# Kernel optimization log

Hardware: AMD Instinct MI355X
Metric: run time of the kernel (lower is better)

The kernel has to match this reference:

```python
import jax, jax.numpy as jnp
import numpy as np

N_TOK = 2048      # flattened batch*seq tokens
D_MODEL = 1024    # in_features
D_INT = 512       # d_intermediate
N_EXPERTS = 8     # n_routed_experts
TOP_K = 2         # n_activated_experts


def setup_inputs() -> dict:
    key = jax.random.key(0)
    k1, k2, k3, k4, k5 = jax.random.split(key, 5)
    x = jax.random.normal(k1, (N_TOK, D_MODEL), dtype=jnp.float32)
    indices = jax.random.randint(k2, (N_TOK, TOP_K), 0, N_EXPERTS, dtype=jnp.int32)
    # router combine weights (normalized over top-k like a softmax router)
    weights = jax.nn.softmax(jax.random.normal(k3, (N_TOK, TOP_K), dtype=jnp.float32), axis=-1)
    # tokens-per-expert counts, consistent with indices (as the router would supply)
    counts = jnp.bincount(indices.reshape(-1), length=N_EXPERTS).astype(jnp.int32)
    # expert weights: fc1 -> 2*d_int (gated MLP), fc2 -> d_model; kaiming-ish scale
    s1 = 1.0 / np.sqrt(D_MODEL)
    s2 = 1.0 / np.sqrt(D_INT)
    fc1_weight = jax.random.uniform(k4, (N_EXPERTS, 2 * D_INT, D_MODEL), jnp.float32, -s1, s1)
    fc2_weight = jax.random.uniform(k5, (N_EXPERTS, D_MODEL, D_INT), jnp.float32, -s2, s2)
    return {"x": x, "weights": weights, "indices": indices, "counts": counts,
            "fc1_weight": fc1_weight, "fc2_weight": fc2_weight}


def reference(x, weights, indices, counts, fc1_weight, fc2_weight):
    # Dense dispatch-free formulation: run every token through every expert's
    # gated MLP, then gather the per-slot expert output. Identical math to the
    # sort / grouped-GEMM / scatter path for the selected (token, expert) pairs.
    # h: (n_tok, n_experts, 2*d_int)
    h = jnp.einsum('td,egd->teg', x, fc1_weight)
    y, z = jnp.split(h, 2, axis=-1)
    a = y * jax.nn.silu(z)  # GatedMLP: y * activation(z)
    # expert outputs: (n_tok, n_experts, d_model)
    out = jnp.einsum('tei,edi->ted', a, fc2_weight)
    # gather the chosen expert output for each of the top-k slots: (n_tok, k, d_model)
    per_slot = jnp.take_along_axis(out, indices[:, :, None], axis=1)
    # combine: z = bmm(weights[:, None], x_by_expert).squeeze(1)
    return jnp.einsum('tk,tkd->td', weights, per_slot)
```

## Files before the change

kernel.cpp:

```cpp
#include <hip/hip_runtime.h>

typedef unsigned short u16;
typedef unsigned int u32;
using short8  = __attribute__((ext_vector_type(8))) short;
using floatx4 = __attribute__((ext_vector_type(4))) float;

#define N_TOK   2048
#define D_MODEL 1024
#define D_INT   512
#define NE      8

#define O_TOK    0
#define O_WROW   24576
#define O_XG     65536
#define O_ACT    10551296
#define O_FC1B   36765696
#define O_FC2B   53542912

static __device__ inline u16 f2bf(float f) {
    u32 u = __builtin_bit_cast(u32, f);
    u = (u + 0x7fffu + ((u >> 16) & 1u)) >> 16;
    return (u16)u;
}
static __device__ inline u32 pack2(float a, float b) {
    return (u32)f2bf(a) | ((u32)f2bf(b) << 16);
}
static __device__ inline void glds16(const u16* g, u16* l) {
    __builtin_amdgcn_global_load_lds(
        (const __attribute__((address_space(1))) void*)g,
        (__attribute__((address_space(3))) void*)l, 16, 0, 0);
}

__global__ __launch_bounds__(256) void prep_kernel(
    const float* __restrict__ x, const float* __restrict__ wts,
    const int* __restrict__ indices, const int* __restrict__ counts,
    const float* __restrict__ fc1, u16* __restrict__ fc1b,
    u16* __restrict__ Xg, int* __restrict__ tok, float* __restrict__ wrow) {
    int b = blockIdx.x, tid = threadIdx.x;
    if (b < 4096) {
        size_t v = (size_t)b * 256 + tid;
        size_t off = v * 8;
        const floatx4* s4 = reinterpret_cast<const floatx4*>(fc1 + off);
        floatx4 a = s4[0], bb = s4[1];
        uint4 o;
        o.x = pack2(a[0], a[1]); o.y = pack2(a[2], a[3]);
        o.z = pack2(bb[0], bb[1]); o.w = pack2(bb[2], bb[3]);
        *reinterpret_cast<uint4*>(fc1b + off) = o;
        return;
    }
    {
        int t = b - 4096;
        int off[NE];
        {
            int acc = 0;
            #pragma unroll
            for (int e = 0; e < NE; e++) { off[e] = acc; acc += ((counts[e] + 63) >> 6) << 6; }
        }
        int e0 = indices[2 * t], e1 = indices[2 * t + 1];
        __shared__ int s0, s1;
        if (tid == 0) { s0 = 0; s1 = 0; }
        __syncthreads();
        int c0 = 0, c1 = 0;
        const int4* ip = reinterpret_cast<const int4*>(indices);
        #pragma unroll
        for (int i = 0; i < 4; i++) {
            int4 vv = ip[tid * 4 + i];
            int q = tid * 16 + i * 4;
            c0 += (q + 0 < 2 * t && vv.x == e0) + (q + 1 < 2 * t && vv.y == e0)
                + (q + 2 < 2 * t && vv.z == e0) + (q + 3 < 2 * t && vv.w == e0);
            c1 += (q + 0 <= 2 * t && vv.x == e1) + (q + 1 <= 2 * t && vv.y == e1)
                + (q + 2 <= 2 * t && vv.z == e1) + (q + 3 <= 2 * t && vv.w == e1);
        }
        if (c0) atomicAdd(&s0, c0);
        if (c1) atomicAdd(&s1, c1);
        __syncthreads();
        int r0 = off[e0] + s0;
        int r1 = off[e1] + s1;
        if (tid == 0) {
            tok[r0] = t; tok[r1] = t;
            wrow[r0] = wts[2 * t]; wrow[r1] = wts[2 * t + 1];
        }
        const floatx4* src = reinterpret_cast<const floatx4*>(x + (size_t)t * D_MODEL);
        floatx4 a = src[tid];
        uint2 o;
        o.x = pack2(a[0], a[1]); o.y = pack2(a[2], a[3]);
        *reinterpret_cast<uint2*>(Xg + (size_t)r0 * D_MODEL + tid * 4) = o;
        *reinterpret_cast<uint2*>(Xg + (size_t)r1 * D_MODEL + tid * 4) = o;
        return;
    }
}

static __device__ inline int xcd_swz576(int bid) {
    return (bid & 7) * 72 + (bid >> 3);
}

__global__ __launch_bounds__(256) void gemm1_kernel(
    const u16* __restrict__ Xg, const u16* __restrict__ fc1b,
    u16* __restrict__ Act, const int* __restrict__ counts,
    const float* __restrict__ fc2, u16* __restrict__ fc2b,
    float* __restrict__ out) {
    __shared__ u16 As[64 * 64];
    __shared__ u16 Bs[128 * 64];
    int tid = threadIdx.x;
    int b = blockIdx.x;
    if (b >= 576) {
        if (b < 2624) {
            size_t v = (size_t)(b - 576) * 256 + tid;
            size_t off = v * 8;
            const floatx4* s4 = reinterpret_cast<const floatx4*>(fc2 + off);
            floatx4 a = s4[0], bb = s4[1];
            uint4 o;
            o.x = pack2(a[0], a[1]); o.y = pack2(a[2], a[3]);
            o.z = pack2(bb[0], bb[1]); o.w = pack2(bb[2], bb[3]);
            *reinterpret_cast<uint4*>(fc2b + off) = o;
        } else {
            int z = b - 2624;
            floatx4* dst = reinterpret_cast<floatx4*>(out) + (size_t)z * 1024;
            #pragma unroll
            for (int i = 0; i < 4; i++) dst[i * 256 + tid] = (floatx4){0.f, 0.f, 0.f, 0.f};
        }
        return;
    }
    int soff[NE + 1];
    {
        int acc = 0;
        #pragma unroll
        for (int e2 = 0; e2 < NE; e2++) { soff[e2] = acc; acc += ((counts[e2] + 63) >> 6) << 6; }
        soff[NE] = acc;
    }
    int t = xcd_swz576(b);
    int bx = t & 7, by = t >> 3;
    int row0 = by * 64;
    if (row0 >= soff[NE]) return;
    int e = 0;
    while (soff[e + 1] <= row0) e++;
    const u16* A  = Xg + (size_t)row0 * 1024;
    const u16* Be = fc1b + (size_t)e * 1024 * 1024;

    int lane = tid & 63, w = tid >> 6;
    int m0 = (w >> 1) * 32, n0 = (w & 1) * 32;
    int lr = lane & 15, kq = lane >> 4;

    const u16* gA[2]; u16* lA[2];
    #pragma unroll
    for (int j = 0; j < 2; j++) {
        int v = tid + j * 256;
        int r = v >> 3, kb = (v & 7) ^ (r & 7);
        gA[j] = A + (size_t)r * 1024 + kb * 8;
        lA[j] = As + (w * 64 + j * 256) * 8;
    }
    const u16* gB[4]; u16* lB[4];
    #pragma unroll
    for (int j = 0; j < 4; j++) {
        int v = tid + j * 256;
        int r = v >> 3, kb = (v & 7) ^ (r & 7);
        int grow = (r < 64) ? (bx * 64 + r) : (448 + bx * 64 + r);
        gB[j] = Be + (size_t)grow * 1024 + kb * 8;
        lB[j] = Bs + (w * 64 + j * 256) * 8;
    }

    floatx4 aY[2][2], aZ[2][2];
    #pragma unroll
    for (int i = 0; i < 2; i++)
        #pragma unroll
        for (int j = 0; j < 2; j++) {
            aY[i][j] = (floatx4){0.f, 0.f, 0.f, 0.f};
            aZ[i][j] = (floatx4){0.f, 0.f, 0.f, 0.f};
        }

    for (int k0 = 0; k0 < 1024; k0 += 64) {
        glds16(gA[0] + k0, lA[0]); glds16(gA[1] + k0, lA[1]);
        glds16(gB[0] + k0, lB[0]); glds16(gB[1] + k0, lB[1]);
        glds16(gB[2] + k0, lB[2]); glds16(gB[3] + k0, lB[3]);
        __syncthreads();
        #pragma unroll
        for (int ks = 0; ks < 2; ks++) {
            int sw = ((ks * 4 + kq) ^ (lr & 7)) * 8;
            short8 af[2], by2[2], bz[2];
            #pragma unroll
            for (int i = 0; i < 2; i++)
                af[i] = *reinterpret_cast<const short8*>(&As[(m0 + i * 16 + lr) * 64 + sw]);
            #pragma unroll
            for (int j = 0; j < 2; j++) {
                by2[j] = *reinterpret_cast<const short8*>(&Bs[(n0 + j * 16 + lr) * 64 + sw]);
                bz[j]  = *reinterpret_cast<const short8*>(&Bs[(64 + n0 + j * 16 + lr) * 64 + sw]);
            }
            #pragma unroll
            for (int i = 0; i < 2; i++)
                #pragma unroll
                for (int j = 0; j < 2; j++) {
                    aY[i][j] = __builtin_amdgcn_mfma_f32_16x16x32_bf16(af[i], by2[j], aY[i][j], 0, 0, 0);
                    aZ[i][j] = __builtin_amdgcn_mfma_f32_16x16x32_bf16(af[i], bz[j], aZ[i][j], 0, 0, 0);
                }
        }
        __syncthreads();
    }
    #pragma unroll
    for (int i = 0; i < 2; i++)
        #pragma unroll
        for (int j = 0; j < 2; j++) {
            floatx4 y = aY[i][j], z = aZ[i][j];
            #pragma unroll
            for (int r = 0; r < 4; r++) {
                float zz = z[r];
                float av = y[r] * (zz / (1.0f + __expf(-zz)));
                int m = m0 + i * 16 + kq * 4 + r;
                int g = bx * 64 + n0 + j * 16 + lr;
                Act[(size_t)(row0 + m) * D_INT + g] = f2bf(av);
            }
        }
}

__global__ __launch_bounds__(256) void gemm2_kernel(
    const u16* __restrict__ Act, const u16* __restrict__ fc2b,
    float* __restrict__ out, const int* __restrict__ counts,
    const int* __restrict__ tok, const float* __restrict__ wrow) {
    __shared__ u16 As[64 * 64];
    __shared__ u16 Bs[128 * 64];
    __shared__ int sTok[64];
    __shared__ float sW[64];
    int tid = threadIdx.x;
    int soff[NE + 1];
    {
        int acc = 0;
        #pragma unroll
        for (int e2 = 0; e2 < NE; e2++) { soff[e2] = acc; acc += ((counts[e2] + 63) >> 6) << 6; }
        soff[NE] = acc;
    }
    int t = xcd_swz576(blockIdx.x);
    int bx = t & 7, by = t >> 3;
    int row0 = by * 64;
    if (row0 >= soff[NE]) return;
    int e = 0;
    while (soff[e + 1] <= row0) e++;
    const u16* A  = Act + (size_t)row0 * 512;
    const u16* Be = fc2b + (size_t)e * 1024 * 512;

    int lane = tid & 63, w = tid >> 6;
    int m0 = (w >> 1) * 32, n0 = (w & 1) * 64;
    int lr = lane & 15, kq = lane >> 4;

    const u16* gA[2]; u16* lA[2];
    #pragma unroll
    for (int j = 0; j < 2; j++) {
        int v = tid + j * 256;
        int r = v >> 3, kb = (v & 7) ^ (r & 7);
        gA[j] = A + (size_t)r * 512 + kb * 8;
        lA[j] = As + (w * 64 + j * 256) * 8;
    }
    const u16* gB[4]; u16* lB[4];
    #pragma unroll
    for (int j = 0; j < 4; j++) {
        int v = tid + j * 256;
        int r = v >> 3, kb = (v & 7) ^ (r & 7);
        gB[j] = Be + (size_t)(bx * 128 + r) * 512 + kb * 8;
        lB[j] = Bs + (w * 64 + j * 256) * 8;
    }

    floatx4 acc[2][4];
    #pragma unroll
    for (int i = 0; i < 2; i++)
        #pragma unroll
        for (int j = 0; j < 4; j++) acc[i][j] = (floatx4){0.f, 0.f, 0.f, 0.f};

    for (int k0 = 0; k0 < 512; k0 += 64) {
        glds16(gA[0] + k0, lA[0]); glds16(gA[1] + k0, lA[1]);
        glds16(gB[0] + k0, lB[0]); glds16(gB[1] + k0, lB[1]);
        glds16(gB[2] + k0, lB[2]); glds16(gB[3] + k0, lB[3]);
        __syncthreads();
        #pragma unroll
        for (int ks = 0; ks < 2; ks++) {
            int sw = ((ks * 4 + kq) ^ (lr & 7)) * 8;
            short8 af[2], bf[4];
            #pragma unroll
            for (int i = 0; i < 2; i++)
                af[i] = *reinterpret_cast<const short8*>(&As[(m0 + i * 16 + lr) * 64 + sw]);
            #pragma unroll
            for (int j = 0; j < 4; j++)
                bf[j] = *reinterpret_cast<const short8*>(&Bs[(n0 + j * 16 + lr) * 64 + sw]);
            #pragma unroll
            for (int i = 0; i < 2; i++)
                #pragma unroll
                for (int j = 0; j < 4; j++)
                    acc[i][j] = __builtin_amdgcn_mfma_f32_16x16x32_bf16(af[i], bf[j], acc[i][j], 0, 0, 0);
        }
        __syncthreads();
    }
    if (tid < 64) {
        int g = row0 + tid;
        bool val = (g - soff[e]) < counts[e];
        sTok[tid] = val ? tok[g] : -1;
        sW[tid]   = val ? wrow[g] : 0.f;
    }
    __syncthreads();
    #pragma unroll
    for (int i = 0; i < 2; i++)
        #pragma unroll
        for (int r = 0; r < 4; r++) {
            int m = m0 + i * 16 + kq * 4 + r;
            int tk = sTok[m];
            if (tk >= 0) {
                float wgt = sW[m];
                float* dst = out + (size_t)tk * D_MODEL + bx * 128;
                #pragma unroll
                for (int j = 0; j < 4; j++)
                    atomicAdd(dst + n0 + j * 16 + lr, wgt * acc[i][j][r]);
            }
        }
}

extern "C" void kernel_launch(void* const* d_in, const int* in_sizes, int n_in,
                              void* d_out, int out_size, void* d_ws, size_t ws_size,
                              hipStream_t stream) {
    const float* x       = (const float*)d_in[0];
    const float* wts     = (const float*)d_in[1];
    const int*   indices = (const int*)d_in[2];
    const int*   counts  = (const int*)d_in[3];
    const float* fc1     = (const float*)d_in[4];
    const float* fc2     = (const float*)d_in[5];
    float* out = (float*)d_out;
    char* ws = (char*)d_ws;

    int*   tok  = (int*)(ws + O_TOK);
    float* wrow = (float*)(ws + O_WROW);
    u16*   Xg   = (u16*)(ws + O_XG);
    u16*   Act  = (u16*)(ws + O_ACT);
    u16*   fc1b = (u16*)(ws + O_FC1B);
    u16*   fc2b = (u16*)(ws + O_FC2B);

    prep_kernel<<<6144, 256, 0, stream>>>(x, wts, indices, counts, fc1, fc1b,
                                          Xg, tok, wrow);
    gemm1_kernel<<<3136, 256, 0, stream>>>(Xg, fc1b, Act, counts, fc2, fc2b, out);
    gemm2_kernel<<<576, 256, 0, stream>>>(Act, fc2b, out, counts, tok, wrow);
}
```

Baseline: 147.2 us.

## Fuse prep, gemm1 and gemm2 into one persistent kernel with grid barriers

Replaces three kernel launches with a single persistent kernel of 576 blocks. The blocks grid-stride through the fc1 conversion and token dispatch, meet at a software grid barrier, run gemm1 while also converting fc2 and zeroing the output, meet at a second barrier, then run gemm2. The aim is to remove launch gaps and tail effects between stages. In exchange it adds a memset, relies on all 576 blocks being resident at once (the barrier deadlocks otherwise), and the barriers can cost more than the launches they replace.

```diff
diff --git a/kernel.cpp b/kernel.cpp
--- a/kernel.cpp
+++ b/kernel.cpp
@@ -9,9 +9,11 @@
 #define D_MODEL 1024
 #define D_INT   512
 #define NE      8
+#define NBLK    576
 
 #define O_TOK    0
 #define O_WROW   24576
+#define O_BAR    45056
 #define O_XG     65536
 #define O_ACT    10551296
 #define O_FC1B   36765696
@@ -31,81 +33,98 @@
         (__attribute__((address_space(3))) void*)l, 16, 0, 0);
 }
 
-__global__ __launch_bounds__(256) void prep_kernel(
+static __device__ inline void grid_barrier(int* c, int nblk) {
+    __syncthreads();
+    if (threadIdx.x == 0) {
+        __threadfence();
+        __hip_atomic_fetch_add(c, 1, __ATOMIC_RELEASE, __HIP_MEMORY_SCOPE_AGENT);
+        while (__hip_atomic_load(c, __ATOMIC_ACQUIRE, __HIP_MEMORY_SCOPE_AGENT) < nblk)
+            __builtin_amdgcn_s_sleep(1);
+        __threadfence();
+    }
+    __syncthreads();
+}
+
+static __device__ inline int xcd_swz576(int bid) {
+    return (bid & 7) * 72 + (bid >> 3);
+}
+
+__global__ __launch_bounds__(256, 4) void moe_fused(
     const float* __restrict__ x, const float* __restrict__ wts,
     const int* __restrict__ indices, const int* __restrict__ counts,
-    const float* __restrict__ fc1, u16* __restrict__ fc1b,
-    u16* __restrict__ Xg, int* __restrict__ tok, float* __restrict__ wrow) {
-    int b = blockIdx.x, tid = threadIdx.x;
-    if (b < 4096) {
-        size_t v = (size_t)b * 256 + tid;
-        size_t off = v * 8;
-        const floatx4* s4 = reinterpret_cast<const floatx4*>(fc1 + off);
-        floatx4 a = s4[0], bb = s4[1];
-        uint4 o;
-        o.x = pack2(a[0], a[1]); o.y = pack2(a[2], a[3]);
-        o.z = pack2(bb[0], bb[1]); o.w = pack2(bb[2], bb[3]);
-        *reinterpret_cast<uint4*>(fc1b + off) = o;
-        return;
-    }
-    {
-        int t = b - 4096;
-        int off[NE];
-        {
-            int acc = 0;
-            #pragma unroll
-            for (int e = 0; e < NE; e++) { off[e] = acc; acc += ((counts[e] + 63) >> 6) << 6; }
-        }
-        int e0 = indices[2 * t], e1 = indices[2 * t + 1];
-        __shared__ int s0, s1;
-        if (tid == 0) { s0 = 0; s1 = 0; }
-        __syncthreads();
-        int c0 = 0, c1 = 0;
-        const int4* ip = reinterpret_cast<const int4*>(indices);
-        #pragma unroll
-        for (int i = 0; i < 4; i++) {
-            int4 vv = ip[tid * 4 + i];
-            int q = tid * 16 + i * 4;
-            c0 += (q + 0 < 2 * t && vv.x == e0) + (q + 1 < 2 * t && vv.y == e0)
-                + (q + 2 < 2 * t && vv.z == e0) + (q + 3 < 2 * t && vv.w == e0);
-            c1 += (q + 0 <= 2 * t && vv.x == e1) + (q + 1 <= 2 * t && vv.y == e1)
-                + (q + 2 <= 2 * t && vv.z == e1) + (q + 3 <= 2 * t && vv.w == e1);
-        }
-        if (c0) atomicAdd(&s0, c0);
-        if (c1) atomicAdd(&s1, c1);
-        __syncthreads();
-        int r0 = off[e0] + s0;
-        int r1 = off[e1] + s1;
-        if (tid == 0) {
-            tok[r0] = t; tok[r1] = t;
-            wrow[r0] = wts[2 * t]; wrow[r1] = wts[2 * t + 1];
-        }
-        const floatx4* src = reinterpret_cast<const floatx4*>(x + (size_t)t * D_MODEL);
-        floatx4 a = src[tid];
-        uint2 o;
-        o.x = pack2(a[0], a[1]); o.y = pack2(a[2], a[3]);
-        *reinterpret_cast<uint2*>(Xg + (size_t)r0 * D_MODEL + tid * 4) = o;
-        *reinterpret_cast<uint2*>(Xg + (size_t)r1 * D_MODEL + tid * 4) = o;
-        return;
-    }
-}
-
-static __device__ inline int xcd_swz576(int bid) {
-    return (bid & 7) * 72 + (bid >> 3);
-}
-
-__global__ __launch_bounds__(256) void gemm1_kernel(
-    const u16* __restrict__ Xg, const u16* __restrict__ fc1b,
-    u16* __restrict__ Act, const int* __restrict__ counts,
-    const float* __restrict__ fc2, u16* __restrict__ fc2b,
-    float* __restrict__ out) {
+    const float* __restrict__ fc1, const float* __restrict__ fc2,
+    u16* __restrict__ fc1b, u16* __restrict__ fc2b,
+    u16* __restrict__ Xg, int* __restrict__ tok, float* __restrict__ wrow,
+    u16* __restrict__ Act, float* __restrict__ out, int* __restrict__ bar) {
     __shared__ u16 As[64 * 64];
     __shared__ u16 Bs[128 * 64];
+    __shared__ int sTok[64];
+    __shared__ float sW[64];
+    __shared__ int s0, s1;
+
     int tid = threadIdx.x;
-    int b = blockIdx.x;
-    if (b >= 576) {
-        if (b < 2624) {
-            size_t v = (size_t)(b - 576) * 256 + tid;
+    int bid = blockIdx.x;
+
+    int soff[NE + 1];
+    {
+        int acc = 0;
+        #pragma unroll
+        for (int e2 = 0; e2 < NE; e2++) { soff[e2] = acc; acc += ((counts[e2] + 63) >> 6) << 6; }
+        soff[NE] = acc;
+    }
+
+    for (int b = bid; b < 6144; b += NBLK) {
+        if (b < 4096) {
+            size_t v = (size_t)b * 256 + tid;
+            size_t off = v * 8;
+            const floatx4* s4 = reinterpret_cast<const floatx4*>(fc1 + off);
+            floatx4 a = s4[0], bb = s4[1];
+            uint4 o;
+            o.x = pack2(a[0], a[1]); o.y = pack2(a[2], a[3]);
+            o.z = pack2(bb[0], bb[1]); o.w = pack2(bb[2], bb[3]);
+            *reinterpret_cast<uint4*>(fc1b + off) = o;
+        } else {
+            int t = b - 4096;
+            int e0 = indices[2 * t], e1 = indices[2 * t + 1];
+            if (tid == 0) { s0 = 0; s1 = 0; }
+            __syncthreads();
+            int c0 = 0, c1 = 0;
+            const int4* ip = reinterpret_cast<const int4*>(indices);
+            #pragma unroll
+            for (int i = 0; i < 4; i++) {
+                int4 vv = ip[tid * 4 + i];
+                int q = tid * 16 + i * 4;
+                c0 += (q + 0 < 2 * t && vv.x == e0) + (q + 1 < 2 * t && vv.y == e0)
+                    + (q + 2 < 2 * t && vv.z == e0) + (q + 3 < 2 * t && vv.w == e0);
+                c1 += (q + 0 <= 2 * t && vv.x == e1) + (q + 1 <= 2 * t && vv.y == e1)
+                    + (q + 2 <= 2 * t && vv.z == e1) + (q + 3 <= 2 * t && vv.w == e1);
+            }
+            if (c0) atomicAdd(&s0, c0);
+            if (c1) atomicAdd(&s1, c1);
+            __syncthreads();
+            int r0 = soff[e0] + s0;
+            int r1 = soff[e1] + s1;
+            if (tid == 0) {
+                tok[r0] = t; tok[r1] = t;
+                wrow[r0] = wts[2 * t]; wrow[r1] = wts[2 * t + 1];
+            }
+            const floatx4* src = reinterpret_cast<const floatx4*>(x + (size_t)t * D_MODEL);
+            floatx4 a = src[tid];
+            uint2 o;
+            o.x = pack2(a[0], a[1]); o.y = pack2(a[2], a[3]);
+            *reinterpret_cast<uint2*>(Xg + (size_t)r0 * D_MODEL + tid * 4) = o;
+            *reinterpret_cast<uint2*>(Xg + (size_t)r1 * D_MODEL + tid * 4) = o;
+        }
+        __syncthreads();
+    }
+    grid_barrier(&bar[0], NBLK);
+
+    int lane = tid & 63, w = tid >> 6;
+    int lr = lane & 15, kq = lane >> 4;
+
+    for (int u = NBLK + bid; u < 3136; u += NBLK) {
+        if (u < 2624) {
+            size_t v = (size_t)(u - 576) * 256 + tid;
             size_t off = v * 8;
             const floatx4* s4 = reinterpret_cast<const floatx4*>(fc2 + off);
             floatx4 a = s4[0], bb = s4[1];
@@ -114,199 +133,175 @@
             o.z = pack2(bb[0], bb[1]); o.w = pack2(bb[2], bb[3]);
             *reinterpret_cast<uint4*>(fc2b + off) = o;
         } else {
-            int z = b - 2624;
+            int z = u - 2624;
             floatx4* dst = reinterpret_cast<floatx4*>(out) + (size_t)z * 1024;
             #pragma unroll
             for (int i = 0; i < 4; i++) dst[i * 256 + tid] = (floatx4){0.f, 0.f, 0.f, 0.f};
         }
-        return;
-    }
-    int soff[NE + 1];
+    }
     {
-        int acc = 0;
-        #pragma unroll
-        for (int e2 = 0; e2 < NE; e2++) { soff[e2] = acc; acc += ((counts[e2] + 63) >> 6) << 6; }
-        soff[NE] = acc;
-    }
-    int t = xcd_swz576(b);
-    int bx = t & 7, by = t >> 3;
-    int row0 = by * 64;
-    if (row0 >= soff[NE]) return;
-    int e = 0;
-    while (soff[e + 1] <= row0) e++;
-    const u16* A  = Xg + (size_t)row0 * 1024;
-    const u16* Be = fc1b + (size_t)e * 1024 * 1024;
-
-    int lane = tid & 63, w = tid >> 6;
-    int m0 = (w >> 1) * 32, n0 = (w & 1) * 32;
-    int lr = lane & 15, kq = lane >> 4;
-
-    const u16* gA[2]; u16* lA[2];
-    #pragma unroll
-    for (int j = 0; j < 2; j++) {
-        int v = tid + j * 256;
-        int r = v >> 3, kb = (v & 7) ^ (r & 7);
-        gA[j] = A + (size_t)r * 1024 + kb * 8;
-        lA[j] = As + (w * 64 + j * 256) * 8;
-    }
-    const u16* gB[4]; u16* lB[4];
-    #pragma unroll
-    for (int j = 0; j < 4; j++) {
-        int v = tid + j * 256;
-        int r = v >> 3, kb = (v & 7) ^ (r & 7);
-        int grow = (r < 64) ? (bx * 64 + r) : (448 + bx * 64 + r);
-        gB[j] = Be + (size_t)grow * 1024 + kb * 8;
-        lB[j] = Bs + (w * 64 + j * 256) * 8;
-    }
-
-    floatx4 aY[2][2], aZ[2][2];
-    #pragma unroll
-    for (int i = 0; i < 2; i++)
-        #pragma unroll
-        for (int j = 0; j < 2; j++) {
-            aY[i][j] = (floatx4){0.f, 0.f, 0.f, 0.f};
-            aZ[i][j] = (floatx4){0.f, 0.f, 0.f, 0.f};
+        int t = xcd_swz576(bid);
+        int bx = t & 7, by = t >> 3;
+        int row0 = by * 64;
+        if (row0 < soff[NE]) {
+            int e = 0;
+            while (soff[e + 1] <= row0) e++;
+            const u16* A  = Xg + (size_t)row0 * 1024;
+            const u16* Be = fc1b + (size_t)e * 1024 * 1024;
+            int m0 = (w >> 1) * 32, n0 = (w & 1) * 32;
+
+            const u16* gA[2]; u16* lA[2];
+            #pragma unroll
+            for (int j = 0; j < 2; j++) {
+                int v = tid + j * 256;
+                int r = v >> 3, kb = (v & 7) ^ (r & 7);
+                gA[j] = A + (size_t)r * 1024 + kb * 8;
+                lA[j] = As + (w * 64 + j * 256) * 8;
+            }
+            const u16* gB[4]; u16* lB[4];
+            #pragma unroll
+            for (int j = 0; j < 4; j++) {
+                int v = tid + j * 256;
+                int r = v >> 3, kb = (v & 7) ^ (r & 7);
+                int grow = (r < 64) ? (bx * 64 + r) : (448 + bx * 64 + r);
+                gB[j] = Be + (size_t)grow * 1024 + kb * 8;
+                lB[j] = Bs + (w * 64 + j * 256) * 8;
+            }
+
+            floatx4 aY[2][2], aZ[2][2];
+            #pragma unroll
+            for (int i = 0; i < 2; i++)
+                #pragma unroll
+                for (int j = 0; j < 2; j++) {
+                    aY[i][j] = (floatx4){0.f, 0.f, 0.f, 0.f};
+                    aZ[i][j] = (floatx4){0.f, 0.f, 0.f, 0.f};
+                }
+
+            for (int k0 = 0; k0 < 1024; k0 += 64) {
+                glds16(gA[0] + k0, lA[0]); glds16(gA[1] + k0, lA[1]);
+                glds16(gB[0] + k0, lB[0]); glds16(gB[1] + k0, lB[1]);
+                glds16(gB[2] + k0, lB[2]); glds16(gB[3] + k0, lB[3]);
+                __syncthreads();
+                #pragma unroll
+                for (int ks = 0; ks < 2; ks++) {
+                    int sw = ((ks * 4 + kq) ^ (lr & 7)) * 8;
+                    short8 af[2], by2[2], bz[2];
+                    #pragma unroll
+                    for (int i = 0; i < 2; i++)
+                        af[i] = *reinterpret_cast<const short8*>(&As[(m0 + i * 16 + lr) * 64 + sw]);
+                    #pragma unroll
+                    for (int j = 0; j < 2; j++) {
+                        by2[j] = *reinterpret_cast<const short8*>(&Bs[(n0 + j * 16 + lr) * 64 + sw]);
+                        bz[j]  = *reinterpret_cast<const short8*>(&Bs[(64 + n0 + j * 16 + lr) * 64 + sw]);
+                    }
+                    #pragma unroll
+                    for (int i = 0; i < 2; i++)
+                        #pragma unroll
+                        for (int j = 0; j < 2; j++) {
+                            aY[i][j] = __builtin_amdgcn_mfma_f32_16x16x32_bf16(af[i], by2[j], aY[i][j], 0, 0, 0);
+                            aZ[i][j] = __builtin_amdgcn_mfma_f32_16x16x32_bf16(af[i], bz[j], aZ[i][j], 0, 0, 0);
+                        }
+                }
+                __syncthreads();
+            }
+            #pragma unroll
+            for (int i = 0; i < 2; i++)
+                #pragma unroll
+                for (int j = 0; j < 2; j++) {
+                    floatx4 y = aY[i][j], z = aZ[i][j];
+                    #pragma unroll
+                    for (int r = 0; r < 4; r++) {
+                        float zz = z[r];
+                        float av = y[r] * (zz / (1.0f + __expf(-zz)));
+                        int m = m0 + i * 16 + kq * 4 + r;
+                        int g = bx * 64 + n0 + j * 16 + lr;
+                        Act[(size_t)(row0 + m) * D_INT + g] = f2bf(av);
+                    }
+                }
         }
-
-    for (int k0 = 0; k0 < 1024; k0 += 64) {
-        glds16(gA[0] + k0, lA[0]); glds16(gA[1] + k0, lA[1]);
-        glds16(gB[0] + k0, lB[0]); glds16(gB[1] + k0, lB[1]);
-        glds16(gB[2] + k0, lB[2]); glds16(gB[3] + k0, lB[3]);
-        __syncthreads();
-        #pragma unroll
-        for (int ks = 0; ks < 2; ks++) {
-            int sw = ((ks * 4 + kq) ^ (lr & 7)) * 8;
-            short8 af[2], by2[2], bz[2];
+    }
+    grid_barrier(&bar[1], NBLK);
+
+    {
+        int t = xcd_swz576(bid);
+        int bx = t & 7, by = t >> 3;
+        int row0 = by * 64;
+        if (row0 < soff[NE]) {
+            int e = 0;
+            while (soff[e + 1] <= row0) e++;
+            const u16* A  = Act + (size_t)row0 * 512;
+            const u16* Be = fc2b + (size_t)e * 1024 * 512;
+            int m0 = (w >> 1) * 32, n0 = (w & 1) * 64;
+
+            const u16* gA[2]; u16* lA[2];
+            #pragma unroll
+            for (int j = 0; j < 2; j++) {
+                int v = tid + j * 256;
+                int r = v >> 3, kb = (v & 7) ^ (r & 7);
+                gA[j] = A + (size_t)r * 512 + kb * 8;
+                lA[j] = As + (w * 64 + j * 256) * 8;
+            }
+            const u16* gB[4]; u16* lB[4];
+            #pragma unroll
+            for (int j = 0; j < 4; j++) {
+                int v = tid + j * 256;
+                int r = v >> 3, kb = (v & 7) ^ (r & 7);
+                gB[j] = Be + (size_t)(bx * 128 + r) * 512 + kb * 8;
+                lB[j] = Bs + (w * 64 + j * 256) * 8;
+            }
+
+            floatx4 acc[2][4];
             #pragma unroll
             for (int i = 0; i < 2; i++)
-                af[i] = *reinterpret_cast<const short8*>(&As[(m0 + i * 16 + lr) * 64 + sw]);
-            #pragma unroll
-            for (int j = 0; j < 2; j++) {
-                by2[j] = *reinterpret_cast<const short8*>(&Bs[(n0 + j * 16 + lr) * 64 + sw]);
-                bz[j]  = *reinterpret_cast<const short8*>(&Bs[(64 + n0 + j * 16 + lr) * 64 + sw]);
-            }
+                #pragma unroll
+                for (int j = 0; j < 4; j++) acc[i][j] = (floatx4){0.f, 0.f, 0.f, 0.f};
+
+            for (int k0 = 0; k0 < 512; k0 += 64) {
+                glds16(gA[0] + k0, lA[0]); glds16(gA[1] + k0, lA[1]);
+                glds16(gB[0] + k0, lB[0]); glds16(gB[1] + k0, lB[1]);
+                glds16(gB[2] + k0, lB[2]); glds16(gB[3] + k0, lB[3]);
+                __syncthreads();
+                #pragma unroll
+                for (int ks = 0; ks < 2; ks++) {
+                    int sw = ((ks * 4 + kq) ^ (lr & 7)) * 8;
+                    short8 af[2], bf[4];
+                    #pragma unroll
+                    for (int i = 0; i < 2; i++)
+                        af[i] = *reinterpret_cast<const short8*>(&As[(m0 + i * 16 + lr) * 64 + sw]);
+                    #pragma unroll
+                    for (int j = 0; j < 4; j++)
+                        bf[j] = *reinterpret_cast<const short8*>(&Bs[(n0 + j * 16 + lr) * 64 + sw]);
+                    #pragma unroll
+                    for (int i = 0; i < 2; i++)
+                        #pragma unroll
+                        for (int j = 0; j < 4; j++)
+                            acc[i][j] = __builtin_amdgcn_mfma_f32_16x16x32_bf16(af[i], bf[j], acc[i][j], 0, 0, 0);
+                }
+                __syncthreads();
+            }
+            if (tid < 64) {
+                int g = row0 + tid;
+                bool val = (g - soff[e]) < counts[e];
+                sTok[tid] = val ? tok[g] : -1;
+                sW[tid]   = val ? wrow[g] : 0.f;
+            }
+            __syncthreads();
             #pragma unroll
             for (int i = 0; i < 2; i++)
                 #pragma unroll
-                for (int j = 0; j < 2; j++) {
-                    aY[i][j] = __builtin_amdgcn_mfma_f32_16x16x32_bf16(af[i], by2[j], aY[i][j], 0, 0, 0);
-                    aZ[i][j] = __builtin_amdgcn_mfma_f32_16x16x32_bf16(af[i], bz[j], aZ[i][j], 0, 0, 0);
+                for (int r = 0; r < 4; r++) {
+                    int m = m0 + i * 16 + kq * 4 + r;
+                    int tk = sTok[m];
+                    if (tk >= 0) {
+                        float wgt = sW[m];
+                        float* dst = out + (size_t)tk * D_MODEL + bx * 128;
+                        #pragma unroll
+                        for (int j = 0; j < 4; j++)
+                            atomicAdd(dst + n0 + j * 16 + lr, wgt * acc[i][j][r]);
+                    }
                 }
         }
-        __syncthreads();
-    }
-    #pragma unroll
-    for (int i = 0; i < 2; i++)
-        #pragma unroll
-        for (int j = 0; j < 2; j++) {
-            floatx4 y = aY[i][j], z = aZ[i][j];
-            #pragma unroll
-            for (int r = 0; r < 4; r++) {
-                float zz = z[r];
-                float av = y[r] * (zz / (1.0f + __expf(-zz)));
-                int m = m0 + i * 16 + kq * 4 + r;
-                int g = bx * 64 + n0 + j * 16 + lr;
-                Act[(size_t)(row0 + m) * D_INT + g] = f2bf(av);
-            }
-        }
-}
-
-__global__ __launch_bounds__(256) void gemm2_kernel(
-    const u16* __restrict__ Act, const u16* __restrict__ fc2b,
-    float* __restrict__ out, const int* __restrict__ counts,
-    const int* __restrict__ tok, const float* __restrict__ wrow) {
-    __shared__ u16 As[64 * 64];
-    __shared__ u16 Bs[128 * 64];
-    __shared__ int sTok[64];
-    __shared__ float sW[64];
-    int tid = threadIdx.x;
-    int soff[NE + 1];
-    {
-        int acc = 0;
-        #pragma unroll
-        for (int e2 = 0; e2 < NE; e2++) { soff[e2] = acc; acc += ((counts[e2] + 63) >> 6) << 6; }
-        soff[NE] = acc;
-    }
-    int t = xcd_swz576(blockIdx.x);
-    int bx = t & 7, by = t >> 3;
-    int row0 = by * 64;
-    if (row0 >= soff[NE]) return;
-    int e = 0;
-    while (soff[e + 1] <= row0) e++;
-    const u16* A  = Act + (size_t)row0 * 512;
-    const u16* Be = fc2b + (size_t)e * 1024 * 512;
-
-    int lane = tid & 63, w = tid >> 6;
-    int m0 = (w >> 1) * 32, n0 = (w & 1) * 64;
-    int lr = lane & 15, kq = lane >> 4;
-
-    const u16* gA[2]; u16* lA[2];
-    #pragma unroll
-    for (int j = 0; j < 2; j++) {
-        int v = tid + j * 256;
-        int r = v >> 3, kb = (v & 7) ^ (r & 7);
-        gA[j] = A + (size_t)r * 512 + kb * 8;
-        lA[j] = As + (w * 64 + j * 256) * 8;
-    }
-    const u16* gB[4]; u16* lB[4];
-    #pragma unroll
-    for (int j = 0; j < 4; j++) {
-        int v = tid + j * 256;
-        int r = v >> 3, kb = (v & 7) ^ (r & 7);
-        gB[j] = Be + (size_t)(bx * 128 + r) * 512 + kb * 8;
-        lB[j] = Bs + (w * 64 + j * 256) * 8;
-    }
-
-    floatx4 acc[2][4];
-    #pragma unroll
-    for (int i = 0; i < 2; i++)
-        #pragma unroll
-        for (int j = 0; j < 4; j++) acc[i][j] = (floatx4){0.f, 0.f, 0.f, 0.f};
-
-    for (int k0 = 0; k0 < 512; k0 += 64) {
-        glds16(gA[0] + k0, lA[0]); glds16(gA[1] + k0, lA[1]);
-        glds16(gB[0] + k0, lB[0]); glds16(gB[1] + k0, lB[1]);
-        glds16(gB[2] + k0, lB[2]); glds16(gB[3] + k0, lB[3]);
-        __syncthreads();
-        #pragma unroll
-        for (int ks = 0; ks < 2; ks++) {
-            int sw = ((ks * 4 + kq) ^ (lr & 7)) * 8;
-            short8 af[2], bf[4];
-            #pragma unroll
-            for (int i = 0; i < 2; i++)
-                af[i] = *reinterpret_cast<const short8*>(&As[(m0 + i * 16 + lr) * 64 + sw]);
-            #pragma unroll
-            for (int j = 0; j < 4; j++)
-                bf[j] = *reinterpret_cast<const short8*>(&Bs[(n0 + j * 16 + lr) * 64 + sw]);
-            #pragma unroll
-            for (int i = 0; i < 2; i++)
-                #pragma unroll
-                for (int j = 0; j < 4; j++)
-                    acc[i][j] = __builtin_amdgcn_mfma_f32_16x16x32_bf16(af[i], bf[j], acc[i][j], 0, 0, 0);
-        }
-        __syncthreads();
-    }
-    if (tid < 64) {
-        int g = row0 + tid;
-        bool val = (g - soff[e]) < counts[e];
-        sTok[tid] = val ? tok[g] : -1;
-        sW[tid]   = val ? wrow[g] : 0.f;
-    }
-    __syncthreads();
-    #pragma unroll
-    for (int i = 0; i < 2; i++)
-        #pragma unroll
-        for (int r = 0; r < 4; r++) {
-            int m = m0 + i * 16 + kq * 4 + r;
-            int tk = sTok[m];
-            if (tk >= 0) {
-                float wgt = sW[m];
-                float* dst = out + (size_t)tk * D_MODEL + bx * 128;
-                #pragma unroll
-                for (int j = 0; j < 4; j++)
-                    atomicAdd(dst + n0 + j * 16 + lr, wgt * acc[i][j][r]);
-            }
-        }
+    }
 }
 
 extern "C" void kernel_launch(void* const* d_in, const int* in_sizes, int n_in,
@@ -323,13 +318,13 @@
 
     int*   tok  = (int*)(ws + O_TOK);
     float* wrow = (float*)(ws + O_WROW);
+    int*   bar  = (int*)(ws + O_BAR);
     u16*   Xg   = (u16*)(ws + O_XG);
     u16*   Act  = (u16*)(ws + O_ACT);
     u16*   fc1b = (u16*)(ws + O_FC1B);
     u16*   fc2b = (u16*)(ws + O_FC2B);
 
-    prep_kernel<<<6144, 256, 0, stream>>>(x, wts, indices, counts, fc1, fc1b,
-                                          Xg, tok, wrow);
-    gemm1_kernel<<<3136, 256, 0, stream>>>(Xg, fc1b, Act, counts, fc2, fc2b, out);
-    gemm2_kernel<<<576, 256, 0, stream>>>(Act, fc2b, out, counts, tok, wrow);
-}
+    hipMemsetAsync(bar, 0, 2 * sizeof(int), stream);
+    moe_fused<<<NBLK, 256, 0, stream>>>(x, wts, indices, counts, fc1, fc2,
+                                        fc1b, fc2b, Xg, tok, wrow, Act, out, bar);
+}
```

After: 359.2 us. +144.0%, slower.

## Gather token rows inside gemm1 instead of materializing grouped X copy

Applied to the files above, without the earlier changes.

The prep kernel now converts x to bf16 in token order with a flat vectorized pass, instead of writing each token's row twice into an expert-sorted buffer. gemm1 looks up the token id for each A-tile row through the tok array and loads directly from the bf16 x. This removes the duplicated scattered writes of the grouped activation buffer. In exchange it adds an indirect tok lookup per row in gemm1 and makes its A loads scattered rather than contiguous.

```diff
diff --git a/kernel.cpp b/kernel.cpp
--- a/kernel.cpp
+++ b/kernel.cpp
@@ -12,7 +12,7 @@
 
 #define O_TOK    0
 #define O_WROW   24576
-#define O_XG     65536
+#define O_XB     65536
 #define O_ACT    10551296
 #define O_FC1B   36765696
 #define O_FC2B   53542912
@@ -35,21 +35,23 @@
     const float* __restrict__ x, const float* __restrict__ wts,
     const int* __restrict__ indices, const int* __restrict__ counts,
     const float* __restrict__ fc1, u16* __restrict__ fc1b,
-    u16* __restrict__ Xg, int* __restrict__ tok, float* __restrict__ wrow) {
+    u16* __restrict__ xb, int* __restrict__ tok, float* __restrict__ wrow) {
     int b = blockIdx.x, tid = threadIdx.x;
-    if (b < 4096) {
+    if (b < 5120) {
         size_t v = (size_t)b * 256 + tid;
-        size_t off = v * 8;
-        const floatx4* s4 = reinterpret_cast<const floatx4*>(fc1 + off);
+        const float* src; u16* dst; size_t off;
+        if (v < 1048576) { src = fc1; dst = fc1b; off = v * 8; }
+        else             { src = x;   dst = xb;   off = (v - 1048576) * 8; }
+        const floatx4* s4 = reinterpret_cast<const floatx4*>(src + off);
         floatx4 a = s4[0], bb = s4[1];
         uint4 o;
         o.x = pack2(a[0], a[1]); o.y = pack2(a[2], a[3]);
         o.z = pack2(bb[0], bb[1]); o.w = pack2(bb[2], bb[3]);
-        *reinterpret_cast<uint4*>(fc1b + off) = o;
+        *reinterpret_cast<uint4*>(dst + off) = o;
         return;
     }
     {
-        int t = b - 4096;
+        int t = b - 5120;
         int off[NE];
         {
             int acc = 0;
@@ -74,18 +76,12 @@
         if (c0) atomicAdd(&s0, c0);
         if (c1) atomicAdd(&s1, c1);
         __syncthreads();
-        int r0 = off[e0] + s0;
-        int r1 = off[e1] + s1;
         if (tid == 0) {
+            int r0 = off[e0] + s0;
+            int r1 = off[e1] + s1;
             tok[r0] = t; tok[r1] = t;
             wrow[r0] = wts[2 * t]; wrow[r1] = wts[2 * t + 1];
         }
-        const floatx4* src = reinterpret_cast<const floatx4*>(x + (size_t)t * D_MODEL);
-        floatx4 a = src[tid];
-        uint2 o;
-        o.x = pack2(a[0], a[1]); o.y = pack2(a[2], a[3]);
-        *reinterpret_cast<uint2*>(Xg + (size_t)r0 * D_MODEL + tid * 4) = o;
-        *reinterpret_cast<uint2*>(Xg + (size_t)r1 * D_MODEL + tid * 4) = o;
         return;
     }
 }
@@ -95,10 +91,10 @@
 }
 
 __global__ __launch_bounds__(256) void gemm1_kernel(
-    const u16* __restrict__ Xg, const u16* __restrict__ fc1b,
+    const u16* __restrict__ xb, const u16* __restrict__ fc1b,
     u16* __restrict__ Act, const int* __restrict__ counts,
     const float* __restrict__ fc2, u16* __restrict__ fc2b,
-    float* __restrict__ out) {
+    float* __restrict__ out, const int* __restrict__ tok) {
     __shared__ u16 As[64 * 64];
     __shared__ u16 Bs[128 * 64];
     int tid = threadIdx.x;
@@ -134,7 +130,6 @@
     if (row0 >= soff[NE]) return;
     int e = 0;
     while (soff[e + 1] <= row0) e++;
-    const u16* A  = Xg + (size_t)row0 * 1024;
     const u16* Be = fc1b + (size_t)e * 1024 * 1024;
 
     int lane = tid & 63, w = tid >> 6;
@@ -146,7 +141,10 @@
     for (int j = 0; j < 2; j++) {
         int v = tid + j * 256;
         int r = v >> 3, kb = (v & 7) ^ (r & 7);
-        gA[j] = A + (size_t)r * 1024 + kb * 8;
+        int g = row0 + r;
+        bool val = (g - soff[e]) < counts[e];
+        int tk = val ? tok[g] : 0;
+        gA[j] = xb + (size_t)tk * 1024 + kb * 8;
         lA[j] = As + (w * 64 + j * 256) * 8;
     }
     const u16* gB[4]; u16* lB[4];
@@ -323,13 +321,14 @@
 
     int*   tok  = (int*)(ws + O_TOK);
     float* wrow = (float*)(ws + O_WROW);
-    u16*   Xg   = (u16*)(ws + O_XG);
+    u16*   xb   = (u16*)(ws + O_XB);
     u16*   Act  = (u16*)(ws + O_ACT);
     u16*   fc1b = (u16*)(ws + O_FC1B);
     u16*   fc2b = (u16*)(ws + O_FC2B);
 
-    prep_kernel<<<6144, 256, 0, stream>>>(x, wts, indices, counts, fc1, fc1b,
-                                          Xg, tok, wrow);
-    gemm1_kernel<<<3136, 256, 0, stream>>>(Xg, fc1b, Act, counts, fc2, fc2b, out);
+    prep_kernel<<<7168, 256, 0, stream>>>(x, wts, indices, counts, fc1, fc1b,
+                                          xb, tok, wrow);
+    gemm1_kernel<<<3136, 256, 0, stream>>>(xb, fc1b, Act, counts, fc2, fc2b,
+                                           out, tok);
     gemm2_kernel<<<576, 256, 0, stream>>>(Act, fc2b, out, counts, tok, wrow);
 }
```

New measurement: 147.0 us. About the same (-0.1%).
